# Kernel tuning notes

Hardware: AMD Instinct MI355X
Metric: run time of the kernel (lower is better)

Reference implementation:

```python
import jax, jax.numpy as jnp
import numpy as np

N_NODES = 100000
N_EDGES = 3200000
IN_SIZE = 256
HID_SIZE = 256
OUT_SIZE = 64


def setup_inputs() -> dict:
    key = jax.random.key(0)
    ks = jax.random.split(key, 8)
    X = jax.random.normal(ks[0], (N_NODES, IN_SIZE), dtype=jnp.float32)
    edge_vals = jax.random.uniform(ks[1], (N_EDGES,), dtype=jnp.float32)
    # xavier-uniform-ish init for weights
    lim1 = float(np.sqrt(6.0 / (IN_SIZE + HID_SIZE)))
    W1 = jax.random.uniform(ks[2], (IN_SIZE, HID_SIZE), minval=-lim1, maxval=lim1, dtype=jnp.float32)
    b1 = jnp.zeros((HID_SIZE,), dtype=jnp.float32)
    lim2 = float(np.sqrt(6.0 / (HID_SIZE + OUT_SIZE)))
    W2 = jax.random.uniform(ks[3], (HID_SIZE, OUT_SIZE), minval=-lim2, maxval=lim2, dtype=jnp.float32)
    b2 = jnp.zeros((OUT_SIZE,), dtype=jnp.float32)
    row = jnp.sort(jax.random.randint(ks[4], (N_EDGES,), 0, N_NODES, dtype=jnp.int32))
    col = jax.random.randint(ks[5], (N_EDGES,), 0, N_NODES, dtype=jnp.int32)
    return {"X": X, "edge_vals": edge_vals, "W1": W1, "b1": b1,
            "W2": W2, "b2": b2, "row": row, "col": col}


def reference(X, edge_vals, W1, b1, W2, b2, row, col):
    """2-layer GCN (eval mode, dropout = identity).

    A is a sparse NxN matrix in COO form: A[row[e], col[e]] = edge_vals[e].
    Layer: relu(A @ (X @ W1) + b1); output: A @ (h @ W2) + b2.
    """
    n = X.shape[0]

    def spmm(dense):  # (A @ dense): gather columns, scale, segment-sum over rows
        gathered = edge_vals[:, None] * dense[col]        # [E, F]
        return jax.ops.segment_sum(gathered, row, num_segments=n)

    h = spmm(X @ W1) + b1          # [N, HID]
    h = jax.nn.relu(h)
    out = spmm(h @ W2) + b2        # [N, OUT]
    return out
```

## Files before the change

### kernel.cpp

```cpp
#include <hip/hip_runtime.h>


constexpr int IN_SIZE = 256;
constexpr int HID = 256;
constexpr int OUTF = 64;

typedef __bf16 bf16x8 __attribute__((ext_vector_type(8)));
typedef float f32x4 __attribute__((ext_vector_type(4)));

__device__ __forceinline__ ushort f2b(float f) {
    uint u = __float_as_uint(f);
    uint r = (u + 0x7fffu + ((u >> 16) & 1u)) >> 16;
    return (ushort)r;
}
__device__ __forceinline__ float b2f(ushort h) {
    return __uint_as_float(((uint)h) << 16);
}

__global__ void setup_kernel(const int* __restrict__ row, int* __restrict__ rp,
                             const float* __restrict__ W1, ushort* __restrict__ W1T,
                             const float* __restrict__ W2, ushort* __restrict__ W2T,
                             int n, int E, int rpB) {
    int b = blockIdx.x;
    if (b < rpB) {
        int i = b * 256 + threadIdx.x;
        if (i > n) return;
        int lo = 0, hi = E;
        while (lo < hi) {
            int mid = (lo + hi) >> 1;
            if (row[mid] < i) lo = mid + 1; else hi = mid;
        }
        rp[i] = lo;
    } else if (b < rpB + 256) {
        int nn = b - rpB;
        int k = threadIdx.x;
        W1T[(size_t)nn * 256 + k] = f2b(W1[(size_t)k * 256 + nn]);
    } else {
        int nn = b - rpB - 256;
        int k = threadIdx.x;
        W2T[(size_t)nn * 256 + k] = f2b(W2[(size_t)k * 64 + nn]);
    }
}

__global__ void prep_edges(const float* __restrict__ vals, const int* __restrict__ col,
                           const float* __restrict__ s, int2* __restrict__ ew,
                           int E, int shift) {
    int e = blockIdx.x * 256 + threadIdx.x;
    if (e >= E) return;
    int c = col[e];
    ew[e] = make_int2(c << shift, __float_as_int(vals[e] * s[c]));
}

__global__ __launch_bounds__(512)
void gemm1_q(const float* __restrict__ A, const ushort* __restrict__ Bt,
             char* __restrict__ Q, float* __restrict__ s1, int M) {
    constexpr int K = 256;
    __shared__ ushort smem[16384];
    __shared__ float red[4][128];
    __shared__ float fin[128];
    ushort* As = smem;
    ushort* Bs = smem + 128 * 40;
    char*   Qs = (char*)smem;
    const int tid = threadIdx.x;
    const int wave = tid >> 6, lane = tid & 63;
    const int quad = lane >> 4, l = lane & 15;
    const int wr = wave >> 2, wc = wave & 3;
    const int m0 = blockIdx.x * 128;

    const int ar = tid >> 2;
    const int ak = (tid & 3) * 8;
    const size_t aoff = (size_t)min(m0 + ar, M - 1) * K + ak;
    const int bn = tid >> 2;
    const int bkp = (tid & 3) * 8;

    f32x4 acc[4][4] = {};

    for (int k0 = 0; k0 < K; k0 += 32) {
        float4 a0 = *(const float4*)(A + aoff + k0);
        float4 a1 = *(const float4*)(A + aoff + k0 + 4);
        uint4 bv0 = *(const uint4*)(Bt + (size_t)bn * K + k0 + bkp);
        uint4 bv1 = *(const uint4*)(Bt + (size_t)(bn + 128) * K + k0 + bkp);
        uint4 pa;
        pa.x = (uint)f2b(a0.x) | ((uint)f2b(a0.y) << 16);
        pa.y = (uint)f2b(a0.z) | ((uint)f2b(a0.w) << 16);
        pa.z = (uint)f2b(a1.x) | ((uint)f2b(a1.y) << 16);
        pa.w = (uint)f2b(a1.z) | ((uint)f2b(a1.w) << 16);
        __syncthreads();
        *(uint4*)&As[ar * 40 + ak] = pa;
        *(uint4*)&Bs[bn * 40 + bkp] = bv0;
        *(uint4*)&Bs[(bn + 128) * 40 + bkp] = bv1;
        __syncthreads();

        bf16x8 af[4], bfr[4];
#pragma unroll
        for (int mt = 0; mt < 4; ++mt)
            af[mt] = *(const bf16x8*)&As[(wr * 64 + mt * 16 + l) * 40 + quad * 8];
#pragma unroll
        for (int nt = 0; nt < 4; ++nt)
            bfr[nt] = *(const bf16x8*)&Bs[(wc * 64 + nt * 16 + l) * 40 + quad * 8];
#pragma unroll
        for (int mt = 0; mt < 4; ++mt)
#pragma unroll
            for (int nt = 0; nt < 4; ++nt)
                acc[mt][nt] = __builtin_amdgcn_mfma_f32_16x16x32_bf16(
                    af[mt], bfr[nt], acc[mt][nt], 0, 0, 0);
    }

    float rmax[4][4];
#pragma unroll
    for (int mt = 0; mt < 4; ++mt)
#pragma unroll
        for (int reg = 0; reg < 4; ++reg) {
            float m = 0.f;
#pragma unroll
            for (int nt = 0; nt < 4; ++nt)
                m = fmaxf(m, fabsf(acc[mt][nt][reg]));
            rmax[mt][reg] = m;
        }
#pragma unroll
    for (int s = 1; s <= 8; s <<= 1)
#pragma unroll
        for (int mt = 0; mt < 4; ++mt)
#pragma unroll
            for (int reg = 0; reg < 4; ++reg)
                rmax[mt][reg] = fmaxf(rmax[mt][reg], __shfl_xor(rmax[mt][reg], s));
    if (l < 4) {
#pragma unroll
        for (int mt = 0; mt < 4; ++mt)
            red[wc][wr * 64 + mt * 16 + quad * 4 + l] = rmax[mt][l];
    }
    __syncthreads();
    if (tid < 128) {
        float m = fmaxf(fmaxf(red[0][tid], red[1][tid]),
                        fmaxf(red[2][tid], red[3][tid]));
        fin[tid] = m;
        int r = m0 + tid;
        if (r < M) s1[r] = m * (1.f / 127.f);
    }
    __syncthreads();

#pragma unroll
    for (int mt = 0; mt < 4; ++mt)
#pragma unroll
        for (int reg = 0; reg < 4; ++reg) {
            int rl = wr * 64 + mt * 16 + quad * 4 + reg;
            float m = fin[rl];
            float inv = m > 0.f ? 127.f / m : 0.f;
#pragma unroll
            for (int nt = 0; nt < 4; ++nt) {
                int c = wc * 64 + nt * 16 + l;
                Qs[rl * 256 + c] = (char)(int)rintf(acc[mt][nt][reg] * inv);
            }
        }
    __syncthreads();

#pragma unroll
    for (int it = 0; it < 4; ++it) {
        int off = it * 8192 + tid * 16;
        int rl = off >> 8;
        if (m0 + rl < M)
            *(uint4*)(Q + (size_t)(m0 + rl) * 256 + (off & 255)) =
                *(const uint4*)(Qs + off);
    }
}

__global__ __launch_bounds__(256, 4)
void gemm2_q(const ushort* __restrict__ A, const ushort* __restrict__ Bt,
             char* __restrict__ Q, float* __restrict__ s2, int M) {
    constexpr int K = 256;
    __shared__ ushort smem[7680];
    __shared__ float red[2][128];
    __shared__ float fin[128];
    ushort* As = smem;
    ushort* Bs = smem + 128 * 40;
    char*   Qs = (char*)smem;
    const int tid = threadIdx.x;
    const int wave = tid >> 6, lane = tid & 63;
    const int quad = lane >> 4, l = lane & 15;
    const int wr = wave >> 1, wc = wave & 1;
    const int m0 = blockIdx.x * 128;

    const int crow = tid >> 2;
    const int cpart = (tid & 3) * 8;
    const size_t aoff0 = (size_t)min(m0 + crow, M - 1) * K + cpart;
    const size_t aoff1 = (size_t)min(m0 + crow + 64, M - 1) * K + cpart;
    const size_t boff  = (size_t)crow * K + cpart;

    f32x4 acc[4][2] = {};

    for (int k0 = 0; k0 < K; k0 += 32) {
        uint4 a0 = *(const uint4*)(A + aoff0 + k0);
        uint4 a1 = *(const uint4*)(A + aoff1 + k0);
        uint4 b0 = *(const uint4*)(Bt + boff + k0);
        __syncthreads();
        *(uint4*)&As[crow * 40 + cpart] = a0;
        *(uint4*)&As[(crow + 64) * 40 + cpart] = a1;
        *(uint4*)&Bs[crow * 40 + cpart] = b0;
        __syncthreads();

        bf16x8 af[4], bfr[2];
        const ushort* ab = &As[(wr * 64 + l) * 40 + quad * 8];
#pragma unroll
        for (int mt = 0; mt < 4; ++mt)
            af[mt] = *(const bf16x8*)(ab + mt * 16 * 40);
        const ushort* bb = &Bs[(wc * 32 + l) * 40 + quad * 8];
#pragma unroll
        for (int nt = 0; nt < 2; ++nt)
            bfr[nt] = *(const bf16x8*)(bb + nt * 16 * 40);
#pragma unroll
        for (int mt = 0; mt < 4; ++mt)
#pragma unroll
            for (int nt = 0; nt < 2; ++nt)
                acc[mt][nt] = __builtin_amdgcn_mfma_f32_16x16x32_bf16(
                    af[mt], bfr[nt], acc[mt][nt], 0, 0, 0);
    }

    float rmax[4][4];
#pragma unroll
    for (int mt = 0; mt < 4; ++mt)
#pragma unroll
        for (int reg = 0; reg < 4; ++reg)
            rmax[mt][reg] = fmaxf(fabsf(acc[mt][0][reg]), fabsf(acc[mt][1][reg]));
#pragma unroll
    for (int s = 1; s <= 8; s <<= 1)
#pragma unroll
        for (int mt = 0; mt < 4; ++mt)
#pragma unroll
            for (int reg = 0; reg < 4; ++reg)
                rmax[mt][reg] = fmaxf(rmax[mt][reg], __shfl_xor(rmax[mt][reg], s));
    if (l < 4) {
#pragma unroll
        for (int mt = 0; mt < 4; ++mt)
            red[wc][wr * 64 + mt * 16 + quad * 4 + l] = rmax[mt][l];
    }
    __syncthreads();
    if (tid < 128) {
        float m = fmaxf(red[0][tid], red[1][tid]);
        fin[tid] = m;
        int r = m0 + tid;
        if (r < M) s2[r] = m * (1.f / 127.f);
    }
    __syncthreads();

#pragma unroll
    for (int mt = 0; mt < 4; ++mt)
#pragma unroll
        for (int reg = 0; reg < 4; ++reg) {
            int rl = wr * 64 + mt * 16 + quad * 4 + reg;
            float m = fin[rl];
            float inv = m > 0.f ? 127.f / m : 0.f;
#pragma unroll
            for (int nt = 0; nt < 2; ++nt) {
                int c = wc * 32 + nt * 16 + l;
                Qs[rl * 64 + c] = (char)(int)rintf(acc[mt][nt][reg] * inv);
            }
        }
    __syncthreads();

#pragma unroll
    for (int it = 0; it < 2; ++it) {
        int off = it * 4096 + tid * 16;
        int rl = off >> 6;
        if (m0 + rl < M)
            *(uint4*)(Q + (size_t)(m0 + rl) * 64 + (off & 63)) =
                *(const uint4*)(Qs + off);
    }
}

__global__ __launch_bounds__(256)
void spmm1_q(const char* __restrict__ Q, const int2* __restrict__ ew,
             const int* __restrict__ rp, const float* __restrict__ bias,
             ushort* __restrict__ H, int n) {
    const int wave = threadIdx.x >> 6;
    const int lane = threadIdx.x & 63;
    const int node = blockIdx.x * 4 + wave;
    if (node >= n) return;
    const int e0 = rp[node], e1 = rp[node + 1];
    float a0 = 0.f, a1 = 0.f, a2 = 0.f, a3 = 0.f;
    int e = e0;
    for (; e + 7 < e1; e += 8) {
#pragma unroll
        for (int u = 0; u < 8; ++u) {
            int2 m = ew[e + u];
            float w = __int_as_float(m.y);
            char4 q = *(const char4*)(Q + (size_t)(uint)m.x + lane * 4);
            a0 += w * (float)q.x;
            a1 += w * (float)q.y;
            a2 += w * (float)q.z;
            a3 += w * (float)q.w;
        }
    }
    for (; e < e1; ++e) {
        int2 m = ew[e];
        float w = __int_as_float(m.y);
        char4 q = *(const char4*)(Q + (size_t)(uint)m.x + lane * 4);
        a0 += w * (float)q.x;
        a1 += w * (float)q.y;
        a2 += w * (float)q.z;
        a3 += w * (float)q.w;
    }
    float4 b = *(const float4*)(bias + lane * 4);
    ushort4 r;
    r.x = f2b(fmaxf(a0 + b.x, 0.f));
    r.y = f2b(fmaxf(a1 + b.y, 0.f));
    r.z = f2b(fmaxf(a2 + b.z, 0.f));
    r.w = f2b(fmaxf(a3 + b.w, 0.f));
    *(ushort4*)(H + (size_t)node * 256 + lane * 4) = r;
}

__global__ __launch_bounds__(256)
void spmm2_q(const char* __restrict__ Q, const int2* __restrict__ ew,
             const int* __restrict__ rp, const float* __restrict__ bias,
             float* __restrict__ O, int n) {
    const int wave = threadIdx.x >> 6;
    const int lane = threadIdx.x & 63;
    const int node = blockIdx.x * 4 + wave;
    if (node >= n) return;
    const int e0 = rp[node], e1 = rp[node + 1];
    float acc = 0.f;
    int e = e0;
    for (; e + 15 < e1; e += 16) {
#pragma unroll
        for (int u = 0; u < 16; ++u) {
            int2 m = ew[e + u];
            acc += __int_as_float(m.y) * (float)Q[(size_t)(uint)m.x + lane];
        }
    }
    for (; e + 3 < e1; e += 4) {
#pragma unroll
        for (int u = 0; u < 4; ++u) {
            int2 m = ew[e + u];
            acc += __int_as_float(m.y) * (float)Q[(size_t)(uint)m.x + lane];
        }
    }
    for (; e < e1; ++e) {
        int2 m = ew[e];
        acc += __int_as_float(m.y) * (float)Q[(size_t)(uint)m.x + lane];
    }
    O[(size_t)node * 64 + lane] = acc + bias[lane];
}

static inline size_t alignup(size_t x) { return (x + 255) & ~(size_t)255; }

extern "C" void kernel_launch(void* const* d_in, const int* in_sizes, int n_in,
                              void* d_out, int out_size, void* d_ws, size_t ws_size,
                              hipStream_t stream) {
    const float* X  = (const float*)d_in[0];
    const float* ev = (const float*)d_in[1];
    const float* W1 = (const float*)d_in[2];
    const float* b1 = (const float*)d_in[3];
    const float* W2 = (const float*)d_in[4];
    const float* b2 = (const float*)d_in[5];
    const int*  row = (const int*)d_in[6];
    const int*  col = (const int*)d_in[7];
    float* out = (float*)d_out;

    const int n = in_sizes[0] / IN_SIZE;
    const int E = in_sizes[1];

    char* p = (char*)d_ws;
    ushort* H    = (ushort*)p; p += alignup((size_t)n * HID * 2);
    char*   Q1   = (char*)p;   p += alignup((size_t)n * HID);
    float*  s1   = (float*)p;  p += alignup((size_t)n * 4);
    char*   Q2   = (char*)p;   p += alignup((size_t)n * OUTF);
    float*  s2   = (float*)p;  p += alignup((size_t)n * 4);
    ushort* W1T  = (ushort*)p; p += alignup((size_t)IN_SIZE * HID * 2);
    ushort* W2T  = (ushort*)p; p += alignup((size_t)HID * OUTF * 2);
    int*    rp   = (int*)p;    p += alignup((size_t)(n + 1) * 4);
    int2*   ewb  = (int2*)p;   p += alignup((size_t)E * 8);

    const int rpB = (n + 1 + 255) / 256;
    setup_kernel<<<rpB + 256 + 64, 256, 0, stream>>>(row, rp, W1, W1T, W2, W2T,
                                                     n, E, rpB);

    gemm1_q<<<(n + 127) / 128, 512, 0, stream>>>(X, W1T, Q1, s1, n);

    prep_edges<<<(E + 255) / 256, 256, 0, stream>>>(ev, col, s1, ewb, E, 8);

    spmm1_q<<<(n + 3) / 4, 256, 0, stream>>>(Q1, ewb, rp, b1, H, n);

    gemm2_q<<<(n + 127) / 128, 256, 0, stream>>>(H, W2T, Q2, s2, n);

    prep_edges<<<(E + 255) / 256, 256, 0, stream>>>(ev, col, s2, ewb, E, 6);

    spmm2_q<<<(n + 3) / 4, 256, 0, stream>>>(Q2, ewb, rp, b2, out, n);
}
```

Before: 472.6 us.

## Split SpMM features into column slices with edge-parallel lanes and shuffle reduction

Both SpMM kernels now split the feature dimension across gridDim.x slices (8 slices of 32 bytes for layer 1, 4 slices of 16 bytes for layer 2). Each wave spreads a node's edges across lane groups and combines the partial sums with xor shuffles, and each wave now handles two nodes. The aim is to make each slice's working set of the quantized feature matrix more cache resident and to get more gathers in flight per wave. In exchange, the edge list and row pointers are re-read once per slice, and each gather is narrower, using only 4 bytes per lane.

```diff
diff --git a/kernel.cpp b/kernel.cpp
--- a/kernel.cpp
+++ b/kernel.cpp
@@ -271,73 +271,85 @@
 void spmm1_q(const char* __restrict__ Q, const int2* __restrict__ ew,
              const int* __restrict__ rp, const float* __restrict__ bias,
              ushort* __restrict__ H, int n) {
+    const int slice = blockIdx.x;
     const int wave = threadIdx.x >> 6;
     const int lane = threadIdx.x & 63;
-    const int node = blockIdx.x * 4 + wave;
-    if (node >= n) return;
-    const int e0 = rp[node], e1 = rp[node + 1];
-    float a0 = 0.f, a1 = 0.f, a2 = 0.f, a3 = 0.f;
-    int e = e0;
-    for (; e + 7 < e1; e += 8) {
-#pragma unroll
-        for (int u = 0; u < 8; ++u) {
-            int2 m = ew[e + u];
+    const int fd = lane & 7;
+    const int es = lane >> 3;
+    const int sliceByte = slice * 32 + fd * 4;
+    float4 b = *(const float4*)(bias + slice * 32 + fd * 4);
+#pragma unroll
+    for (int nd = 0; nd < 2; ++nd) {
+        const int node = (blockIdx.y * 4 + wave) * 2 + nd;
+        if (node >= n) continue;
+        const int e0 = rp[node], e1 = rp[node + 1];
+        float a0 = 0.f, a1 = 0.f, a2 = 0.f, a3 = 0.f;
+        for (int e = e0 + es; e < e1; e += 8) {
+            int2 m = ew[e];
             float w = __int_as_float(m.y);
-            char4 q = *(const char4*)(Q + (size_t)(uint)m.x + lane * 4);
+            char4 q = *(const char4*)(Q + (size_t)(uint)m.x + sliceByte);
             a0 += w * (float)q.x;
             a1 += w * (float)q.y;
             a2 += w * (float)q.z;
             a3 += w * (float)q.w;
         }
-    }
-    for (; e < e1; ++e) {
-        int2 m = ew[e];
-        float w = __int_as_float(m.y);
-        char4 q = *(const char4*)(Q + (size_t)(uint)m.x + lane * 4);
-        a0 += w * (float)q.x;
-        a1 += w * (float)q.y;
-        a2 += w * (float)q.z;
-        a3 += w * (float)q.w;
-    }
-    float4 b = *(const float4*)(bias + lane * 4);
-    ushort4 r;
-    r.x = f2b(fmaxf(a0 + b.x, 0.f));
-    r.y = f2b(fmaxf(a1 + b.y, 0.f));
-    r.z = f2b(fmaxf(a2 + b.z, 0.f));
-    r.w = f2b(fmaxf(a3 + b.w, 0.f));
-    *(ushort4*)(H + (size_t)node * 256 + lane * 4) = r;
+#pragma unroll
+        for (int s = 8; s <= 32; s <<= 1) {
+            a0 += __shfl_xor(a0, s);
+            a1 += __shfl_xor(a1, s);
+            a2 += __shfl_xor(a2, s);
+            a3 += __shfl_xor(a3, s);
+        }
+        if (es == 0) {
+            ushort4 r;
+            r.x = f2b(fmaxf(a0 + b.x, 0.f));
+            r.y = f2b(fmaxf(a1 + b.y, 0.f));
+            r.z = f2b(fmaxf(a2 + b.z, 0.f));
+            r.w = f2b(fmaxf(a3 + b.w, 0.f));
+            *(ushort4*)(H + (size_t)node * 256 + slice * 32 + fd * 4) = r;
+        }
+    }
 }
 
 __global__ __launch_bounds__(256)
 void spmm2_q(const char* __restrict__ Q, const int2* __restrict__ ew,
              const int* __restrict__ rp, const float* __restrict__ bias,
              float* __restrict__ O, int n) {
+    const int slice = blockIdx.x;
     const int wave = threadIdx.x >> 6;
     const int lane = threadIdx.x & 63;
-    const int node = blockIdx.x * 4 + wave;
-    if (node >= n) return;
-    const int e0 = rp[node], e1 = rp[node + 1];
-    float acc = 0.f;
-    int e = e0;
-    for (; e + 15 < e1; e += 16) {
-#pragma unroll
-        for (int u = 0; u < 16; ++u) {
-            int2 m = ew[e + u];
-            acc += __int_as_float(m.y) * (float)Q[(size_t)(uint)m.x + lane];
-        }
-    }
-    for (; e + 3 < e1; e += 4) {
-#pragma unroll
-        for (int u = 0; u < 4; ++u) {
-            int2 m = ew[e + u];
-            acc += __int_as_float(m.y) * (float)Q[(size_t)(uint)m.x + lane];
-        }
-    }
-    for (; e < e1; ++e) {
-        int2 m = ew[e];
-        acc += __int_as_float(m.y) * (float)Q[(size_t)(uint)m.x + lane];
-    }
-    O[(size_t)node * 64 + lane] = acc + bias[lane];
+    const int fd = lane & 3;
+    const int es = lane >> 2;
+    const int sliceByte = slice * 16 + fd * 4;
+    float4 b = *(const float4*)(bias + slice * 16 + fd * 4);
+#pragma unroll
+    for (int nd = 0; nd < 2; ++nd) {
+        const int node = (blockIdx.y * 4 + wave) * 2 + nd;
+        if (node >= n) continue;
+        const int e0 = rp[node], e1 = rp[node + 1];
+        float a0 = 0.f, a1 = 0.f, a2 = 0.f, a3 = 0.f;
+        for (int e = e0 + es; e < e1; e += 16) {
+            int2 m = ew[e];
+            float w = __int_as_float(m.y);
+            char4 q = *(const char4*)(Q + (size_t)(uint)m.x + sliceByte);
+            a0 += w * (float)q.x;
+            a1 += w * (float)q.y;
+            a2 += w * (float)q.z;
+            a3 += w * (float)q.w;
+        }
+#pragma unroll
+        for (int s = 4; s <= 32; s <<= 1) {
+            a0 += __shfl_xor(a0, s);
+            a1 += __shfl_xor(a1, s);
+            a2 += __shfl_xor(a2, s);
+            a3 += __shfl_xor(a3, s);
+        }
+        if (es == 0) {
+            float4 r;
+            r.x = a0 + b.x; r.y = a1 + b.y; r.z = a2 + b.z; r.w = a3 + b.w;
+            *(float4*)(O + (size_t)node * 64 + slice * 16 + fd * 4) = r;
+        }
+    }
 }
 
 static inline size_t alignup(size_t x) { return (x + 255) & ~(size_t)255; }
@@ -377,11 +389,17 @@
 
     prep_edges<<<(E + 255) / 256, 256, 0, stream>>>(ev, col, s1, ewb, E, 8);
 
-    spmm1_q<<<(n + 3) / 4, 256, 0, stream>>>(Q1, ewb, rp, b1, H, n);
+    {
+        dim3 g(8, (n + 7) / 8);
+        spmm1_q<<<g, 256, 0, stream>>>(Q1, ewb, rp, b1, H, n);
+    }
 
     gemm2_q<<<(n + 127) / 128, 256, 0, stream>>>(H, W2T, Q2, s2, n);
 
     prep_edges<<<(E + 255) / 256, 256, 0, stream>>>(ev, col, s2, ewb, E, 6);
 
-    spmm2_q<<<(n + 3) / 4, 256, 0, stream>>>(Q2, ewb, rp, b2, out, n);
-}
+    {
+        dim3 g(4, (n + 7) / 8);
+        spmm2_q<<<g, 256, 0, stream>>>(Q2, ewb, rp, b2, out, n);
+    }
+}
```

Result: slower. 829.2 us (+75.4%).

## Bucket-sort each row's edges by column range to improve gather locality

Applied to the files above, without the earlier changes.

Adds a per-node counting sort that groups each row's edges into 16 buckets by column high bits, so the SpMM gathers in a warp touch nearby feature rows at the same time. The sorted column and value arrays then feed the edge-prep kernels. This adds a serial per-thread pass over each row's edges with divergent loops and extra global traffic, on top of the existing prep work. Its aim is better L2 hit rates in the gathers.

```diff
diff --git a/kernel.cpp b/kernel.cpp
--- a/kernel.cpp
+++ b/kernel.cpp
@@ -42,13 +42,34 @@
     }
 }
 
-__global__ void prep_edges(const float* __restrict__ vals, const int* __restrict__ col,
+__global__ void sort_edges(const int* __restrict__ col, const float* __restrict__ vals,
+                           const int* __restrict__ rp, int* __restrict__ scol,
+                           float* __restrict__ sval, int n, int shift) {
+    int node = blockIdx.x * 256 + threadIdx.x;
+    if (node >= n) return;
+    int e0 = rp[node], e1 = rp[node + 1];
+    int cnt[16] = {};
+    for (int e = e0; e < e1; ++e) cnt[(uint)col[e] >> shift]++;
+    int off[16];
+    int acc = 0;
+#pragma unroll
+    for (int b = 0; b < 16; ++b) { off[b] = acc; acc += cnt[b]; }
+    for (int e = e0; e < e1; ++e) {
+        int c = col[e];
+        int b = (uint)c >> shift;
+        int pos = e0 + off[b]++;
+        scol[pos] = c;
+        sval[pos] = vals[e];
+    }
+}
+
+__global__ void prep_edges(const float* __restrict__ sval, const int* __restrict__ scol,
                            const float* __restrict__ s, int2* __restrict__ ew,
-                           int E, int shift) {
+                           int E, int shiftQ) {
     int e = blockIdx.x * 256 + threadIdx.x;
     if (e >= E) return;
-    int c = col[e];
-    ew[e] = make_int2(c << shift, __float_as_int(vals[e] * s[c]));
+    int c = scol[e];
+    ew[e] = make_int2(c << shiftQ, __float_as_int(sval[e] * s[c]));
 }
 
 __global__ __launch_bounds__(512)
@@ -367,21 +388,29 @@
     ushort* W1T  = (ushort*)p; p += alignup((size_t)IN_SIZE * HID * 2);
     ushort* W2T  = (ushort*)p; p += alignup((size_t)HID * OUTF * 2);
     int*    rp   = (int*)p;    p += alignup((size_t)(n + 1) * 4);
+    int*    scol = (int*)p;    p += alignup((size_t)E * 4);
+    float*  sval = (float*)p;  p += alignup((size_t)E * 4);
     int2*   ewb  = (int2*)p;   p += alignup((size_t)E * 8);
 
     const int rpB = (n + 1 + 255) / 256;
     setup_kernel<<<rpB + 256 + 64, 256, 0, stream>>>(row, rp, W1, W1T, W2, W2T,
                                                      n, E, rpB);
 
+    int bits = 0;
+    while ((1 << bits) < n) ++bits;
+    int shift = bits > 4 ? bits - 4 : 0;
+
+    sort_edges<<<(n + 255) / 256, 256, 0, stream>>>(col, ev, rp, scol, sval, n, shift);
+
     gemm1_q<<<(n + 127) / 128, 512, 0, stream>>>(X, W1T, Q1, s1, n);
 
-    prep_edges<<<(E + 255) / 256, 256, 0, stream>>>(ev, col, s1, ewb, E, 8);
+    prep_edges<<<(E + 255) / 256, 256, 0, stream>>>(sval, scol, s1, ewb, E, 8);
 
     spmm1_q<<<(n + 3) / 4, 256, 0, stream>>>(Q1, ewb, rp, b1, H, n);
 
     gemm2_q<<<(n + 127) / 128, 256, 0, stream>>>(H, W2T, Q2, s2, n);
 
-    prep_edges<<<(E + 255) / 256, 256, 0, stream>>>(ev, col, s2, ewb, E, 6);
+    prep_edges<<<(E + 255) / 256, 256, 0, stream>>>(sval, scol, s2, ewb, E, 6);
 
     spmm2_q<<<(n + 3) / 4, 256, 0, stream>>>(Q2, ewb, rp, b2, out, n);
 }
```

After: 597.9 us. 26.5% more time.
